# Kernel optimization log

Hardware: AMD Instinct MI355X
Metric: run time of the kernel (lower is better)

Reference implementation:

```python
import jax, jax.numpy as jnp
import numpy as np
import math


def setup_inputs() -> dict:
    key = jax.random.key(0)
    ks = jax.random.split(key, 8)
    B, S, dim = 4, 1024, 2048
    H, D = 16, 128          # n_heads = dim // core_dim
    T = 1024                # cached kv length
    w_scale = 1.0 / math.sqrt(dim)
    return {
        "x": jax.random.normal(ks[0], (B, S, dim), dtype=jnp.float32),
        "k_cache": jax.random.normal(ks[1], (B, H, T, D), dtype=jnp.float32),
        "v_cache": jax.random.normal(ks[2], (B, H, T, D), dtype=jnp.float32),
        "Wq": jax.random.normal(ks[3], (dim, dim), dtype=jnp.float32) * w_scale,
        "bq": jnp.zeros((dim,), jnp.float32),
        "Wk": jax.random.normal(ks[4], (dim, dim), dtype=jnp.float32) * w_scale,
        "bk": jnp.zeros((dim,), jnp.float32),
        "Wv": jax.random.normal(ks[5], (dim, dim), dtype=jnp.float32) * w_scale,
        "bv": jnp.zeros((dim,), jnp.float32),
        "Wo": jax.random.normal(ks[6], (dim, dim), dtype=jnp.float32) * w_scale,
        "bo": jnp.zeros((dim,), jnp.float32),
    }


def _split_heads(t, H):
    # [B, S, dim] -> [B, H, S, D]
    B, S, dim = t.shape
    return t.reshape(B, S, H, dim // H).transpose(0, 2, 1, 3)


def reference(x, k_cache, v_cache, Wq, bq, Wk, bk, Wv, bv, Wo, bo):
    B, S, dim = x.shape
    H = k_cache.shape[1]
    D = dim // H
    T = k_cache.shape[2]

    q = _split_heads(x @ Wq.T + bq, H)                 # [B,H,S,D]
    k_new = _split_heads(x @ Wk.T + bk, H)             # [B,H,S,D]
    v_new = _split_heads(x @ Wv.T + bv, H)

    k = jnp.concatenate([k_cache, k_new], axis=2)      # [B,H,T+S,D]
    v = jnp.concatenate([v_cache, v_new], axis=2)

    scale = 1.0 / math.sqrt(D)
    scores = jnp.einsum("bhqd,bhkd->bhqk", q, k) * scale   # [B,H,S,T+S]

    # causal mask with cache offset: query i may attend to key j iff j <= i + T
    q_pos = jnp.arange(S)[:, None] + T
    k_pos = jnp.arange(T + S)[None, :]
    mask = k_pos <= q_pos                              # [S, T+S]
    scores = jnp.where(mask[None, None], scores, jnp.finfo(scores.dtype).min)

    attn = jax.nn.softmax(scores, axis=-1)
    ctx = jnp.einsum("bhqk,bhkd->bhqd", attn, v)       # [B,H,S,D]
    ctx = ctx.transpose(0, 2, 1, 3).reshape(B, S, dim) # merge heads

    out = ctx @ Wo.T + bo                              # dropout is identity (p=0 / eval)
    return (out, k, v)
```

## Files before the change

kernel.cpp:

```cpp
#include <hip/hip_runtime.h>
#include <hip/hip_bf16.h>

typedef float f32x4 __attribute__((ext_vector_type(4)));
typedef __bf16 bf16x8 __attribute__((ext_vector_type(8)));
typedef unsigned short u16x8 __attribute__((ext_vector_type(8)));

#define DIMK 2048
#define QSCALE ((float)(0.08838834764831845 * 1.4426950408889634))

__device__ __forceinline__ unsigned short f2bf(float f) {
    union { float f; unsigned int u; } v; v.f = f;
    unsigned int r = v.u + 0x7fffu + ((v.u >> 16) & 1u);
    return (unsigned short)(r >> 16);
}
__device__ __forceinline__ float bf2f(unsigned short u) {
    union { unsigned int i; float f; } v; v.i = ((unsigned int)u) << 16; return v.f;
}

__device__ __forceinline__ void lds_load16(void* lds, const void* gsrc) {
    __builtin_amdgcn_global_load_lds(
        (const __attribute__((address_space(1))) unsigned int*)gsrc,
        (__attribute__((address_space(3))) unsigned int*)lds,
        16, 0, 0);
}


__global__ __launch_bounds__(256) void conv_all(
    const float* __restrict__ x,  const float* __restrict__ Wq,
    const float* __restrict__ Wk, const float* __restrict__ Wv,
    const float* __restrict__ Wo,
    unsigned short* __restrict__ xbf, unsigned short* __restrict__ Wqb,
    unsigned short* __restrict__ Wkb, unsigned short* __restrict__ Wvb,
    unsigned short* __restrict__ Wob)
{
    int i = blockIdx.x * 256 + threadIdx.x;
    const float* src; unsigned short* dst; size_t off;
    if (i < 2097152) { src = x; dst = xbf; off = i; }
    else {
        int j = (i - 2097152) >> 20;
        off = (size_t)((i - 2097152) & 1048575);
        src = j == 0 ? Wq : j == 1 ? Wk : j == 2 ? Wv : Wo;
        dst = j == 0 ? Wqb : j == 1 ? Wkb : j == 2 ? Wvb : Wob;
    }
    f32x4 v = *(const f32x4*)(src + off * 4);
    ushort4 pk = { f2bf(v[0]), f2bf(v[1]), f2bf(v[2]), f2bf(v[3]) };
    *(ushort4*)(dst + off * 4) = pk;
}

__global__ __launch_bounds__(256) void k_dual(
    const float* __restrict__ kc, float* __restrict__ kout, unsigned short* __restrict__ Kbf)
{
    size_t i4 = (size_t)blockIdx.x * 256 + threadIdx.x;
    size_t e = i4 * 4;
    size_t bh = e >> 17, rem = e & 131071;
    f32x4 v = *(const f32x4*)(kc + e);
    size_t dsto = (bh << 18) + rem;
    *(f32x4*)(kout + dsto) = v;
    ushort4 pk = { f2bf(v[0]), f2bf(v[1]), f2bf(v[2]), f2bf(v[3]) };
    *(ushort4*)(Kbf + dsto) = pk;
}

__global__ __launch_bounds__(256) void v_dual(
    const float* __restrict__ vc, float* __restrict__ vout, unsigned short* __restrict__ Vtb)
{
    __shared__ unsigned short T[128 * 72];
    const int kv0 = blockIdx.x * 64;
    const int bh = blockIdx.y;
    const int tid = threadIdx.x;
    const float* src = vc + ((size_t)bh << 17) + (size_t)kv0 * 128;
    float* vdst = vout + ((size_t)bh << 18) + (size_t)kv0 * 128;
    #pragma unroll
    for (int r = 0; r < 8; ++r) {
        int e4 = r * 256 + tid;
        int kv = e4 >> 5, d0 = (e4 & 31) << 2;
        f32x4 v = *(const f32x4*)(src + kv * 128 + d0);
        *(f32x4*)(vdst + kv * 128 + d0) = v;
        #pragma unroll
        for (int i = 0; i < 4; ++i) T[(d0 + i) * 72 + kv] = f2bf(v[i]);
    }
    __syncthreads();
    #pragma unroll
    for (int r = 0; r < 8; ++r) {
        int e = r * 256 + tid;
        int d = e >> 4, k4 = (e & 15) << 2;
        ushort4 pk = { T[d * 72 + k4], T[d * 72 + k4 + 1], T[d * 72 + k4 + 2], T[d * 72 + k4 + 3] };
        *(ushort4*)(Vtb + ((size_t)bh * 128 + d) * 2048 + kv0 + k4) = pk;
    }
}


#define GQ_TILE(T, VMC, DO_STAGE)                                                   \
    {                                                                               \
        const int bo = (T) & 3;                                                     \
        const unsigned short* la = LA + bo * 8192;                                  \
        const unsigned short* lb = LB + bo * 8192;                                  \
        bf16x8 af[4], bfj[4];                                                       \
        _Pragma("unroll")                                                           \
        for (int i = 0; i < 4; ++i)                                                 \
            af[i] = *(const bf16x8*)(la + (wr * 128 + i * 16 + c) * 32 + eoff);     \
        _Pragma("unroll")                                                           \
        for (int j = 0; j < 4; ++j)                                                 \
            bfj[j] = *(const bf16x8*)(lb + (wc * 64 + j * 16 + c) * 32 + eoff);     \
        if (DO_STAGE) {                                                             \
            const int sb = ((T) + 3) & 3;                                           \
            lds_load16(LA + sb * 8192 + w * 512, Asrc + ((T) + 3) * 32);            \
            lds_load16(LA + sb * 8192 + 4096 + w * 512, Asrc2 + ((T) + 3) * 32);    \
        }                                                                           \
        asm volatile("s_waitcnt lgkmcnt(0)" ::: "memory");                          \
        __builtin_amdgcn_sched_barrier(0);                                          \
        __builtin_amdgcn_s_setprio(1);                                              \
        _Pragma("unroll")                                                           \
        for (int i = 0; i < 4; ++i)                                                 \
            _Pragma("unroll")                                                       \
            for (int j = 0; j < 4; ++j)                                             \
                acc[i][j] = __builtin_amdgcn_mfma_f32_16x16x32_bf16(af[i], bfj[j], acc[i][j], 0, 0, 0); \
        __builtin_amdgcn_s_setprio(0);                                              \
        _Pragma("unroll")                                                           \
        for (int i = 0; i < 4; ++i)                                                 \
            af[i] = *(const bf16x8*)(la + (wr * 128 + 64 + i * 16 + c) * 32 + eoff);\
        if (DO_STAGE) {                                                             \
            const int sb = ((T) + 3) & 3;                                           \
            lds_load16(LB + sb * 8192 + w * 512, Bsrc + ((T) + 3) * 32);            \
            lds_load16(LB + sb * 8192 + 4096 + w * 512, Bsrc2 + ((T) + 3) * 32);    \
        }                                                                           \
        asm volatile("s_waitcnt vmcnt(" #VMC ")" ::: "memory");                     \
        asm volatile("s_waitcnt lgkmcnt(0)" ::: "memory");                          \
        __builtin_amdgcn_s_barrier();                                               \
        __builtin_amdgcn_sched_barrier(0);                                          \
        __builtin_amdgcn_s_setprio(1);                                              \
        _Pragma("unroll")                                                           \
        for (int i = 0; i < 4; ++i)                                                 \
            _Pragma("unroll")                                                       \
            for (int j = 0; j < 4; ++j)                                             \
                acc[4 + i][j] = __builtin_amdgcn_mfma_f32_16x16x32_bf16(af[i], bfj[j], acc[4 + i][j], 0, 0, 0); \
        __builtin_amdgcn_s_setprio(0);                                              \
    }

__device__ __forceinline__ void gemm_core256(
    const unsigned short* __restrict__ A16, const unsigned short* __restrict__ W16,
    int m0, int n0, unsigned short* LA, unsigned short* LB, f32x4 (&acc)[8][4],
    int tid, int w, int wr, int wc, int g, int c)
{
    const int srow = tid >> 2;
    const int achk = (tid & 3) ^ ((tid >> 3) & 3);
    const unsigned short* Asrc  = A16 + (size_t)(m0 + srow) * DIMK + achk * 8;
    const unsigned short* Asrc2 = A16 + (size_t)(m0 + 128 + srow) * DIMK + achk * 8;
    const unsigned short* Bsrc  = W16 + (size_t)(n0 + srow) * DIMK + achk * 8;
    const unsigned short* Bsrc2 = W16 + (size_t)(n0 + 128 + srow) * DIMK + achk * 8;
    const int eoff = (g ^ ((c >> 1) & 3)) * 8;

    #pragma unroll
    for (int ts = 0; ts < 3; ++ts) {
        lds_load16(LA + ts * 8192 + w * 512, Asrc + ts * 32);
        lds_load16(LA + ts * 8192 + 4096 + w * 512, Asrc2 + ts * 32);
        lds_load16(LB + ts * 8192 + w * 512, Bsrc + ts * 32);
        lds_load16(LB + ts * 8192 + 4096 + w * 512, Bsrc2 + ts * 32);
    }
    asm volatile("s_waitcnt vmcnt(8)" ::: "memory");
    __builtin_amdgcn_s_barrier();

    #pragma unroll 4
    for (int t = 0; t < 61; ++t)
        GQ_TILE(t, 8, true);
    GQ_TILE(61, 4, false);
    GQ_TILE(62, 0, false);
    GQ_TILE(63, 0, false);
}

__global__ __launch_bounds__(512, 2) void gemm_qkv256(
    const unsigned short* __restrict__ xbf,
    const unsigned short* __restrict__ Wqb, const unsigned short* __restrict__ Wkb,
    const unsigned short* __restrict__ Wvb,
    const float* __restrict__ bq, const float* __restrict__ bk, const float* __restrict__ bv,
    unsigned short* __restrict__ Qbf,
    float* __restrict__ kout, unsigned short* __restrict__ Kbf,
    float* __restrict__ vout, unsigned short* __restrict__ Vtb)
{
    const int o = blockIdx.x;
    const int xcd = o & 7;
    const int local = o >> 3;
    const int nloc = local >> 4;
    const int mblk = local & 15;
    const int nblk = xcd * 3 + nloc;
    const int m0 = mblk * 256;
    const int n0g = nblk * 256;
    const int mi = n0g >> 11;
    const int n0 = n0g & 2047;

    const unsigned short* W16 = mi == 0 ? Wqb : (mi == 1 ? Wkb : Wvb);
    const float* bias = mi == 0 ? bq : (mi == 1 ? bk : bv);

    const int tid = threadIdx.x;
    const int lane = tid & 63;
    const int w = tid >> 6;
    const int g = lane >> 4;
    const int c = lane & 15;
    const int wr = w >> 2, wc = w & 3;

    __shared__ unsigned short LA[4 * 8192];
    __shared__ unsigned short LB[4 * 8192];

    f32x4 acc[8][4];
    #pragma unroll
    for (int i = 0; i < 8; ++i)
        #pragma unroll
        for (int j = 0; j < 4; ++j)
            acc[i][j] = f32x4{0.f, 0.f, 0.f, 0.f};

    gemm_core256(xbf, W16, m0, n0, LA, LB, acc, tid, w, wr, wc, g, c);

    #pragma unroll
    for (int j = 0; j < 4; ++j) {
        const int n = n0 + wc * 64 + j * 16 + c;
        const float bn = bias[n];
        const int hh = n >> 7, d = n & 127;
        #pragma unroll
        for (int i = 0; i < 8; ++i) {
            float y4[4];
            #pragma unroll
            for (int tq = 0; tq < 4; ++tq) y4[tq] = acc[i][j][tq] + bn;
            const int mb = m0 + wr * 128 + i * 16 + g * 4;
            if (mi == 0) {
                #pragma unroll
                for (int tq = 0; tq < 4; ++tq) {
                    int m = mb + tq; int b = m >> 10, s = m & 1023;
                    Qbf[((((size_t)b * 16 + hh) << 10) + s) * 128 + d] = f2bf(y4[tq] * QSCALE);
                }
            } else if (mi == 1) {
                #pragma unroll
                for (int tq = 0; tq < 4; ++tq) {
                    int m = mb + tq; int b = m >> 10, s = m & 1023;
                    kout[(((size_t)b * 16 + hh) * 2048 + 1024 + s) * 128 + d] = y4[tq];
                    Kbf[(((size_t)b * 16 + hh) << 18) + (size_t)(1024 + s) * 128 + d] = f2bf(y4[tq]);
                }
            } else {
                #pragma unroll
                for (int tq = 0; tq < 4; ++tq) {
                    int m = mb + tq; int b = m >> 10, s = m & 1023;
                    vout[(((size_t)b * 16 + hh) * 2048 + 1024 + s) * 128 + d] = y4[tq];
                }
                int b = mb >> 10, s = mb & 1023;
                ushort4 pk = { f2bf(y4[0]), f2bf(y4[1]), f2bf(y4[2]), f2bf(y4[3]) };
                *(ushort4*)(Vtb + (((size_t)b * 16 + hh) * 128 + d) * 2048 + 1024 + s) = pk;
            }
        }
    }
}

__global__ __launch_bounds__(512, 2) void gemm_wo256(
    const unsigned short* __restrict__ ctx, const unsigned short* __restrict__ Wob,
    const float* __restrict__ bo, float* __restrict__ outp)
{
    const int o = blockIdx.x;
    const int xcd = o & 7;
    const int mblk = o >> 3;
    const int m0 = mblk * 256;
    const int n0 = xcd * 256;

    const int tid = threadIdx.x;
    const int lane = tid & 63;
    const int w = tid >> 6;
    const int g = lane >> 4;
    const int c = lane & 15;
    const int wr = w >> 2, wc = w & 3;

    __shared__ unsigned short LA[4 * 8192];
    __shared__ unsigned short LB[4 * 8192];

    f32x4 acc[8][4];
    #pragma unroll
    for (int i = 0; i < 8; ++i)
        #pragma unroll
        for (int j = 0; j < 4; ++j)
            acc[i][j] = f32x4{0.f, 0.f, 0.f, 0.f};

    gemm_core256(ctx, Wob, m0, n0, LA, LB, acc, tid, w, wr, wc, g, c);

    #pragma unroll
    for (int j = 0; j < 4; ++j) {
        const int n = n0 + wc * 64 + j * 16 + c;
        const float bn = bo[n];
        #pragma unroll
        for (int i = 0; i < 8; ++i) {
            const int mb = m0 + wr * 128 + i * 16 + g * 4;
            #pragma unroll
            for (int tq = 0; tq < 4; ++tq)
                outp[(size_t)(mb + tq) * 2048 + n] = acc[i][j][tq] + bn;
        }
    }
}

__global__ __launch_bounds__(256) void attn5(
    const unsigned short* __restrict__ Qbf,
    const unsigned short* __restrict__ Kbf,
    const unsigned short* __restrict__ Vtb,
    unsigned short* __restrict__ Pp,
    float* __restrict__ Mp,
    float* __restrict__ Lp)
{
    const int o = blockIdx.x;
    const int xcd = o & 7;
    const int kk0 = o >> 3;
    const int half = kk0 & 1;
    const int qt = 7 - ((kk0 >> 1) & 7);
    const int bh = (kk0 >> 4) * 8 + xcd;

    const int tid = threadIdx.x;
    const int lane = tid & 63;
    const int w = tid >> 6;
    const int g = lane >> 4;
    const int c = lane & 15;
    const int cswz = (c & 7) << 3;

    __shared__ unsigned short Ks[2][64 * 128];
    __shared__ unsigned short Vs[2][128 * 64];

    const unsigned short* Qb = Qbf + ((size_t)bh * 1024 + qt * 128) * 128;
    const unsigned short* Kb = Kbf + ((size_t)bh << 18);
    const unsigned short* Vt = Vtb + ((size_t)bh << 18);

    bf16x8 aq[2][4];
    #pragma unroll
    for (int m2 = 0; m2 < 2; ++m2)
        #pragma unroll
        for (int kd = 0; kd < 4; ++kd)
            aq[m2][kd] = *(const bf16x8*)(Qb + (w * 32 + m2 * 16 + c) * 128 + kd * 32 + g * 8);

    f32x4 od[2][8];
    #pragma unroll
    for (int m2 = 0; m2 < 2; ++m2)
        #pragma unroll
        for (int nf = 0; nf < 8; ++nf)
            od[m2][nf] = f32x4{0.f, 0.f, 0.f, 0.f};
    float mrow[2] = { -1e30f, -1e30f };
    float lrow[2] = { 0.f, 0.f };

    const int krow = tid >> 4;
    const int kswz = (((tid & 15) << 4) ^ ((krow & 7) << 4)) >> 1;
    const unsigned short* Kl = Kb + (size_t)krow * 128 + kswz;

    const int vd = tid >> 3;
    const int ck = tid & 7;
    const int kkv = ck >> 2;
    const int av = (ck >> 1) & 1;
    const int p0 = kkv * 32 + (((2 * ck) & 3) << 3) + av * 4;
    const int p1 = kkv * 32 + (((2 * ck + 1) & 3) << 3) + av * 4;

    const int cnt = 9 + qt;
    const int t0 = half * cnt;
    const int lim_min = 1024 + qt * 128 + w * 32;

    u16x8 vreg0, vreg1, vreg2, vreg3;

    {
        const int kv0 = t0 * 64;
        #pragma unroll
        for (int r = 0; r < 4; ++r)
            lds_load16(&Ks[0][w * 512 + r * 2048], Kl + (size_t)(kv0 + r * 16) * 128);
        vreg0 = *(const u16x8*)(Vt + (size_t)(vd +  0) * 2048 + kv0 + ck * 8);
        vreg1 = *(const u16x8*)(Vt + (size_t)(vd + 32) * 2048 + kv0 + ck * 8);
        vreg2 = *(const u16x8*)(Vt + (size_t)(vd + 64) * 2048 + kv0 + ck * 8);
        vreg3 = *(const u16x8*)(Vt + (size_t)(vd + 96) * 2048 + kv0 + ck * 8);
        #pragma unroll
        for (int r = 0; r < 4; ++r) {
            const int d = vd + r * 32;
            const int sw = (d & 7) << 3;
            unsigned short* row = &Vs[0][d * 64];
            u16x8 vv = r == 0 ? vreg0 : r == 1 ? vreg1 : r == 2 ? vreg2 : vreg3;
            ushort4 lo = { vv[0], vv[1], vv[2], vv[3] };
            ushort4 hi = { vv[4], vv[5], vv[6], vv[7] };
            *(ushort4*)(&row[p0 ^ sw]) = lo;
            *(ushort4*)(&row[p1 ^ sw]) = hi;
        }
        __syncthreads();
    }

    int cur = 0;
    for (int t = t0; t < t0 + cnt; ++t) {
        const int kv0 = t * 64;
        const bool next = (t + 1 < t0 + cnt);

        if (next) {
            const int kvn = kv0 + 64;
            #pragma unroll
            for (int r = 0; r < 4; ++r)
                lds_load16(&Ks[cur ^ 1][w * 512 + r * 2048], Kl + (size_t)(kvn + r * 16) * 128);
            vreg0 = *(const u16x8*)(Vt + (size_t)(vd +  0) * 2048 + kvn + ck * 8);
            vreg1 = *(const u16x8*)(Vt + (size_t)(vd + 32) * 2048 + kvn + ck * 8);
            vreg2 = *(const u16x8*)(Vt + (size_t)(vd + 64) * 2048 + kvn + ck * 8);
            vreg3 = *(const u16x8*)(Vt + (size_t)(vd + 96) * 2048 + kvn + ck * 8);
        }

        const unsigned short* Ksc = &Ks[cur][0];
        const unsigned short* Vsc = &Vs[cur][0];

        f32x4 sc[2][4];
        #pragma unroll
        for (int m2 = 0; m2 < 2; ++m2)
            #pragma unroll
            for (int n = 0; n < 4; ++n)
                sc[m2][n] = f32x4{0.f, 0.f, 0.f, 0.f};
        #pragma unroll
        for (int kd = 0; kd < 4; ++kd) {
            bf16x8 bk[4];
            #pragma unroll
            for (int n = 0; n < 4; ++n)
                bk[n] = *(const bf16x8*)(&Ksc[(n * 16 + c) * 128 + ((kd * 32 + g * 8) ^ cswz)]);
            #pragma unroll
            for (int m2 = 0; m2 < 2; ++m2)
                #pragma unroll
                for (int n = 0; n < 4; ++n)
                    sc[m2][n] = __builtin_amdgcn_mfma_f32_16x16x32_bf16(bk[n], aq[m2][kd], sc[m2][n], 0, 0, 0);
        }

        const bool need_mask = (kv0 + 63 > lim_min);
        #pragma unroll
        for (int m2 = 0; m2 < 2; ++m2) {
            if (need_mask) {
                const int lim = lim_min + m2 * 16 + c;
                #pragma unroll
                for (int n = 0; n < 4; ++n)
                    #pragma unroll
                    for (int j = 0; j < 4; ++j)
                        if (kv0 + n * 16 + g * 4 + j > lim) sc[m2][n][j] = -1e30f;
            }
            float rmax = sc[m2][0][0];
            #pragma unroll
            for (int n = 0; n < 4; ++n)
                #pragma unroll
                for (int j = 0; j < 4; ++j)
                    rmax = fmaxf(rmax, sc[m2][n][j]);
            rmax = fmaxf(rmax, __shfl_xor(rmax, 16));
            rmax = fmaxf(rmax, __shfl_xor(rmax, 32));

            if (!__all(rmax <= mrow[m2] + 8.0f)) {
                const float mnew = fmaxf(mrow[m2], rmax);
                const float fs = exp2f(mrow[m2] - mnew);
                mrow[m2] = mnew;
                lrow[m2] *= fs;
                #pragma unroll
                for (int j = 0; j < 4; ++j) {
                    const float fsj = __shfl(fs, (lane & 48) | (g * 4 + j));
                    #pragma unroll
                    for (int nf = 0; nf < 8; ++nf)
                        od[m2][nf][j] *= fsj;
                }
            }
            const float mm = mrow[m2];
            float rsum = 0.f;
            #pragma unroll
            for (int n = 0; n < 4; ++n)
                #pragma unroll
                for (int j = 0; j < 4; ++j) {
                    float p = exp2f(sc[m2][n][j] - mm);
                    sc[m2][n][j] = p;
                    rsum += p;
                }
            rsum += __shfl_xor(rsum, 16);
            rsum += __shfl_xor(rsum, 32);
            lrow[m2] += rsum;
        }

        if (next) {
            unsigned short* Vn = &Vs[cur ^ 1][0];
            #pragma unroll
            for (int r = 0; r < 4; ++r) {
                const int d = vd + r * 32;
                const int sw = (d & 7) << 3;
                unsigned short* row = &Vn[d * 64];
                u16x8 vv = r == 0 ? vreg0 : r == 1 ? vreg1 : r == 2 ? vreg2 : vreg3;
                ushort4 lo = { vv[0], vv[1], vv[2], vv[3] };
                ushort4 hi = { vv[4], vv[5], vv[6], vv[7] };
                *(ushort4*)(&row[p0 ^ sw]) = lo;
                *(ushort4*)(&row[p1 ^ sw]) = hi;
            }
        }

        union PA { u16x8 u; bf16x8 b; };
        PA pa[2][2];
        #pragma unroll
        for (int m2 = 0; m2 < 2; ++m2)
            #pragma unroll
            for (int kk = 0; kk < 2; ++kk)
                #pragma unroll
                for (int e = 0; e < 8; ++e)
                    pa[m2][kk].u[e] = f2bf(sc[m2][2 * kk + (e >> 2)][e & 3]);

        #pragma unroll
        for (int kk = 0; kk < 2; ++kk) {
            #pragma unroll
            for (int nf = 0; nf < 8; ++nf) {
                bf16x8 bv = *(const bf16x8*)(&Vsc[(nf * 16 + c) * 64 + ((kk * 32 + g * 8) ^ cswz)]);
                od[0][nf] = __builtin_amdgcn_mfma_f32_16x16x32_bf16(pa[0][kk].b, bv, od[0][nf], 0, 0, 0);
                od[1][nf] = __builtin_amdgcn_mfma_f32_16x16x32_bf16(pa[1][kk].b, bv, od[1][nf], 0, 0, 0);
            }
        }

        __syncthreads();
        cur ^= 1;
    }

    const size_t pbase = ((size_t)(half * 64 + bh) * 1024 + qt * 128) * 128;
    const int mlbase = (half * 64 + bh) * 1024 + qt * 128;
    if (lane < 16) {
        #pragma unroll
        for (int m2 = 0; m2 < 2; ++m2) {
            Mp[mlbase + w * 32 + m2 * 16 + c] = mrow[m2];
            Lp[mlbase + w * 32 + m2 * 16 + c] = lrow[m2];
        }
    }
    #pragma unroll
    for (int m2 = 0; m2 < 2; ++m2) {
        #pragma unroll
        for (int j = 0; j < 4; ++j) {
            const float lj = __shfl(lrow[m2], (lane & 48) | (g * 4 + j));
            const float rl = 1.0f / lj;
            const int ql = w * 32 + m2 * 16 + g * 4 + j;
            #pragma unroll
            for (int nf = 0; nf < 8; ++nf)
                Pp[pbase + (size_t)ql * 128 + nf * 16 + c] = f2bf(od[m2][nf][j] * rl);
        }
    }
}

__global__ __launch_bounds__(256) void merge_ctx(
    const unsigned short* __restrict__ Pp, const float* __restrict__ Mp,
    const float* __restrict__ Lp, unsigned short* __restrict__ ctx)
{
    const int idx = blockIdx.x * 256 + threadIdx.x;
    const int r = idx >> 4;
    const int dc = (idx & 15) << 3;
    const float m0 = Mp[r], m1 = Mp[65536 + r];
    const float l0 = Lp[r], l1 = Lp[65536 + r];
    const float M = fmaxf(m0, m1);
    float w0 = l0 * exp2f(m0 - M);
    float w1 = l1 * exp2f(m1 - M);
    const float inv = 1.0f / (w0 + w1);
    w0 *= inv; w1 *= inv;
    u16x8 a = *(const u16x8*)(Pp + (size_t)r * 128 + dc);
    u16x8 bb = *(const u16x8*)(Pp + (size_t)8388608 + (size_t)r * 128 + dc);
    const int bh = r >> 10, q = r & 1023;
    unsigned short* dst = ctx + ((size_t)(bh >> 4) * 1024 + q) * 2048 + (bh & 15) * 128 + dc;
    u16x8 outv;
    #pragma unroll
    for (int e = 0; e < 8; ++e)
        outv[e] = f2bf(w0 * bf2f(a[e]) + w1 * bf2f(bb[e]));
    *(u16x8*)dst = outv;
}

__global__ __launch_bounds__(256) void copy_cache(
    const float* __restrict__ kc, const float* __restrict__ vc,
    float* __restrict__ kout, float* __restrict__ vout)
{
    size_t i4 = (size_t)blockIdx.x * 256 + threadIdx.x;
    const float* src = blockIdx.y ? vc : kc;
    float* dst = blockIdx.y ? vout : kout;
    size_t e = i4 * 4;
    size_t bh = e >> 17, rem = e & 131071;
    f32x4 v = *(const f32x4*)(src + e);
    *(f32x4*)(dst + (bh << 18) + rem) = v;
}

template<int MODE, bool ABF16>
__global__ __launch_bounds__(256) void gemm_bt(
    const void* __restrict__ Ag, const float* __restrict__ Wf,
    const float* __restrict__ bias, void* __restrict__ dst)
{
    const int tid = threadIdx.x;
    const int lane = tid & 63;
    const int w = tid >> 6;
    const int g = lane >> 4;
    const int c = lane & 15;
    const int wr = w >> 1, wc = w & 1;
    const int m0 = blockIdx.y * 128;
    const int n0 = blockIdx.x * 128;

    __shared__ unsigned short As[128 * 40];
    __shared__ unsigned short Bs[128 * 40];

    f32x4 acc[4][4];
    #pragma unroll
    for (int i = 0; i < 4; ++i)
        #pragma unroll
        for (int j = 0; j < 4; ++j)
            acc[i][j] = f32x4{0.f, 0.f, 0.f, 0.f};

    for (int k0 = 0; k0 < DIMK; k0 += 32) {
        __syncthreads();
        if constexpr (ABF16) {
            const unsigned short* A16 = (const unsigned short*)Ag;
            #pragma unroll
            for (int r = 0; r < 2; ++r) {
                int e8 = r * 256 + tid;
                int row = e8 >> 2, col = (e8 & 3) << 3;
                *(uint4*)(&As[row * 40 + col]) =
                    *(const uint4*)(A16 + (size_t)(m0 + row) * DIMK + k0 + col);
            }
        } else {
            const float* Af = (const float*)Ag;
            #pragma unroll
            for (int r = 0; r < 4; ++r) {
                int e4 = r * 256 + tid;
                int row = e4 >> 3, col = (e4 & 7) << 2;
                f32x4 v = *(const f32x4*)(Af + (size_t)(m0 + row) * DIMK + k0 + col);
                ushort4 pk = { f2bf(v[0]), f2bf(v[1]), f2bf(v[2]), f2bf(v[3]) };
                *(ushort4*)(&As[row * 40 + col]) = pk;
            }
        }
        {
            #pragma unroll
            for (int r = 0; r < 4; ++r) {
                int e4 = r * 256 + tid;
                int row = e4 >> 3, col = (e4 & 7) << 2;
                f32x4 v = *(const f32x4*)(Wf + (size_t)(n0 + row) * DIMK + k0 + col);
                ushort4 pk = { f2bf(v[0]), f2bf(v[1]), f2bf(v[2]), f2bf(v[3]) };
                *(ushort4*)(&Bs[row * 40 + col]) = pk;
            }
        }
        __syncthreads();

        bf16x8 af[4], bfr[4];
        #pragma unroll
        for (int i = 0; i < 4; ++i)
            af[i] = *(const bf16x8*)(&As[(wr * 64 + i * 16 + c) * 40 + g * 8]);
        #pragma unroll
        for (int i = 0; i < 4; ++i)
            bfr[i] = *(const bf16x8*)(&Bs[(wc * 64 + i * 16 + c) * 40 + g * 8]);
        #pragma unroll
        for (int i = 0; i < 4; ++i)
            #pragma unroll
            for (int j = 0; j < 4; ++j)
                acc[i][j] = __builtin_amdgcn_mfma_f32_16x16x32_bf16(af[i], bfr[j], acc[i][j], 0, 0, 0);
    }

    #pragma unroll
    for (int j = 0; j < 4; ++j) {
        const int n = n0 + wc * 64 + j * 16 + c;
        const float bn = bias[n];
        #pragma unroll
        for (int i = 0; i < 4; ++i) {
            float y4[4];
            #pragma unroll
            for (int tq = 0; tq < 4; ++tq) y4[tq] = acc[i][j][tq] + bn;
            const int mb = m0 + wr * 64 + i * 16 + g * 4;
            if constexpr (MODE == 0) {
                #pragma unroll
                for (int tq = 0; tq < 4; ++tq) {
                    int m = mb + tq; int b = m >> 10, s = m & 1023;
                    int hh = n >> 7, d = n & 127;
                    ((unsigned short*)dst)[((((size_t)b * 16 + hh) << 10) + s) * 128 + d] = f2bf(y4[tq] * QSCALE);
                }
            } else if constexpr (MODE == 1) {
                #pragma unroll
                for (int tq = 0; tq < 4; ++tq) {
                    int m = mb + tq; int b = m >> 10, s = m & 1023;
                    int hh = n >> 7, d = n & 127;
                    ((float*)dst)[(((size_t)b * 16 + hh) * 2048 + 1024 + s) * 128 + d] = y4[tq];
                }
            } else {
                #pragma unroll
                for (int tq = 0; tq < 4; ++tq)
                    ((float*)dst)[(size_t)(mb + tq) * 2048 + n] = y4[tq];
            }
        }
    }
}

__global__ __launch_bounds__(256) void attn_stage(
    const unsigned short* __restrict__ Qbf,
    const float* __restrict__ Kf, const float* __restrict__ Vf,
    unsigned short* __restrict__ ctx)
{
    const int qt = blockIdx.x;
    const int bh = blockIdx.y;
    const int b = bh >> 4, h = bh & 15;
    const int tid = threadIdx.x;
    const int lane = tid & 63;
    const int w = tid >> 6;
    const int g = lane >> 4;
    const int c = lane & 15;

    __shared__ unsigned short Ksl[64 * 136];
    __shared__ unsigned short Vtl[128 * 72];
    __shared__ unsigned short Ps[4 * 32 * 72];

    bf16x8 aq[2][4];
    const unsigned short* Qb = Qbf + ((size_t)bh * 1024 + qt * 128) * 128;
    #pragma unroll
    for (int m2 = 0; m2 < 2; ++m2)
        #pragma unroll
        for (int kk = 0; kk < 4; ++kk)
            aq[m2][kk] = *(const bf16x8*)(Qb + (w * 32 + m2 * 16 + c) * 128 + kk * 32 + g * 8);

    f32x4 od[2][8];
    #pragma unroll
    for (int m2 = 0; m2 < 2; ++m2)
        #pragma unroll
        for (int nf = 0; nf < 8; ++nf)
            od[m2][nf] = f32x4{0.f, 0.f, 0.f, 0.f};
    float mrow[2][4], lrow[2][4];
    #pragma unroll
    for (int m2 = 0; m2 < 2; ++m2)
        #pragma unroll
        for (int j = 0; j < 4; ++j) { mrow[m2][j] = -1e30f; lrow[m2][j] = 0.f; }

    const float* Kb = Kf + (size_t)bh * 2048 * 128;
    const float* Vb = Vf + (size_t)bh * 2048 * 128;
    const int ntiles = 18 + 2 * qt;

    for (int t = 0; t < ntiles; ++t) {
        __syncthreads();
        const float* Kt = Kb + (size_t)t * 64 * 128;
        #pragma unroll
        for (int r = 0; r < 8; ++r) {
            int e4 = r * 256 + tid;
            int kv = e4 >> 5, d0 = (e4 & 31) << 2;
            f32x4 v = *(const f32x4*)(Kt + kv * 128 + d0);
            ushort4 pk = { f2bf(v[0]), f2bf(v[1]), f2bf(v[2]), f2bf(v[3]) };
            *(ushort4*)(&Ksl[kv * 136 + d0]) = pk;
        }
        const float* Vg = Vb + (size_t)t * 64 * 128;
        #pragma unroll
        for (int r = 0; r < 8; ++r) {
            int e4 = tid * 8 + r;
            int kv = e4 >> 5, d0 = (e4 & 31) << 2;
            f32x4 v = *(const f32x4*)(Vg + kv * 128 + d0);
            #pragma unroll
            for (int i = 0; i < 4; ++i)
                Vtl[(d0 + i) * 72 + kv] = f2bf(v[i]);
        }
        __syncthreads();

        f32x4 sc[2][4];
        #pragma unroll
        for (int m2 = 0; m2 < 2; ++m2)
            #pragma unroll
            for (int n = 0; n < 4; ++n)
                sc[m2][n] = f32x4{0.f, 0.f, 0.f, 0.f};
        #pragma unroll
        for (int kk = 0; kk < 4; ++kk) {
            bf16x8 bk[4];
            #pragma unroll
            for (int n = 0; n < 4; ++n)
                bk[n] = *(const bf16x8*)(&Ksl[(n * 16 + c) * 136 + kk * 32 + g * 8]);
            #pragma unroll
            for (int m2 = 0; m2 < 2; ++m2)
                #pragma unroll
                for (int n = 0; n < 4; ++n)
                    sc[m2][n] = __builtin_amdgcn_mfma_f32_16x16x32_bf16(aq[m2][kk], bk[n], sc[m2][n], 0, 0, 0);
        }

        const int kvbase = t * 64;
        #pragma unroll
        for (int m2 = 0; m2 < 2; ++m2) {
            #pragma unroll
            for (int j = 0; j < 4; ++j) {
                const int qg = qt * 128 + w * 32 + m2 * 16 + g * 4 + j;
                const int lim = qg + 1024;
                float rmax = -1e30f;
                #pragma unroll
                for (int n = 0; n < 4; ++n) {
                    float s = sc[m2][n][j] * QSCALE;
                    if (kvbase + n * 16 + c > lim) s = -1e30f;
                    sc[m2][n][j] = s;
                    rmax = fmaxf(rmax, s);
                }
                #pragma unroll
                for (int off = 1; off < 16; off <<= 1)
                    rmax = fmaxf(rmax, __shfl_xor(rmax, off));
                float mold = mrow[m2][j];
                float mnew = fmaxf(mold, rmax);
                mrow[m2][j] = mnew;
                float fs = exp2f(mold - mnew);
                float rsum = 0.f;
                #pragma unroll
                for (int n = 0; n < 4; ++n) {
                    float p = exp2f(sc[m2][n][j] - mnew);
                    sc[m2][n][j] = p;
                    rsum += p;
                }
                #pragma unroll
                for (int off = 1; off < 16; off <<= 1)
                    rsum += __shfl_xor(rsum, off);
                lrow[m2][j] = lrow[m2][j] * fs + rsum;
                #pragma unroll
                for (int nf = 0; nf < 8; ++nf)
                    od[m2][nf][j] *= fs;
            }
        }

        unsigned short* Pw = &Ps[w * 32 * 72];
        #pragma unroll
        for (int m2 = 0; m2 < 2; ++m2)
            #pragma unroll
            for (int n = 0; n < 4; ++n)
                #pragma unroll
                for (int j = 0; j < 4; ++j)
                    Pw[(m2 * 16 + g * 4 + j) * 72 + n * 16 + c] = f2bf(sc[m2][n][j]);

        #pragma unroll
        for (int kk = 0; kk < 2; ++kk) {
            bf16x8 ap0 = *(const bf16x8*)(&Ps[(w * 32 + c) * 72 + kk * 32 + g * 8]);
            bf16x8 ap1 = *(const bf16x8*)(&Ps[(w * 32 + 16 + c) * 72 + kk * 32 + g * 8]);
            #pragma unroll
            for (int nf = 0; nf < 8; ++nf) {
                bf16x8 bv = *(const bf16x8*)(&Vtl[(nf * 16 + c) * 72 + kk * 32 + g * 8]);
                od[0][nf] = __builtin_amdgcn_mfma_f32_16x16x32_bf16(ap0, bv, od[0][nf], 0, 0, 0);
                od[1][nf] = __builtin_amdgcn_mfma_f32_16x16x32_bf16(ap1, bv, od[1][nf], 0, 0, 0);
            }
        }
    }

    #pragma unroll
    for (int m2 = 0; m2 < 2; ++m2) {
        #pragma unroll
        for (int j = 0; j < 4; ++j) {
            const int qg = qt * 128 + w * 32 + m2 * 16 + g * 4 + j;
            const float rl = 1.0f / lrow[m2][j];
            #pragma unroll
            for (int nf = 0; nf < 8; ++nf) {
                const int d = nf * 16 + c;
                ctx[((size_t)b * 1024 + qg) * 2048 + h * 128 + d] = f2bf(od[m2][nf][j] * rl);
            }
        }
    }
}

extern "C" void kernel_launch(void* const* d_in, const int* in_sizes, int n_in,
                              void* d_out, int out_size, void* d_ws, size_t ws_size,
                              hipStream_t stream) {
    const float* x  = (const float*)d_in[0];
    const float* kc = (const float*)d_in[1];
    const float* vc = (const float*)d_in[2];
    const float* Wq = (const float*)d_in[3];
    const float* bq = (const float*)d_in[4];
    const float* Wk = (const float*)d_in[5];
    const float* bk = (const float*)d_in[6];
    const float* Wv = (const float*)d_in[7];
    const float* bv = (const float*)d_in[8];
    const float* Wo = (const float*)d_in[9];
    const float* bo = (const float*)d_in[10];

    float* outp = (float*)d_out;
    float* kout = outp + (size_t)8388608;
    float* vout = outp + (size_t)25165824;

    unsigned short* Qbf = (unsigned short*)d_ws;
    unsigned short* ctx = Qbf + (size_t)8388608;
    unsigned short* Kbf = ctx + (size_t)8388608;
    unsigned short* Vtb = Kbf + (size_t)16777216;
    unsigned short* xbf = Vtb + (size_t)16777216;
    unsigned short* Wqb = xbf + (size_t)8388608;
    unsigned short* Wkb = Wqb + (size_t)4194304;
    unsigned short* Wvb = Wkb + (size_t)4194304;
    unsigned short* Wob = Wvb + (size_t)4194304;
    unsigned short* Pp = xbf;
    float* Mp = (float*)Wvb;
    float* Lp = Mp + (size_t)131072;

    const bool full = ws_size >= (size_t)150994944;

    if (full) {
        conv_all<<<24576, 256, 0, stream>>>(x, Wq, Wk, Wv, Wo, xbf, Wqb, Wkb, Wvb, Wob);
        k_dual<<<8192, 256, 0, stream>>>(kc, kout, Kbf);
        v_dual<<<dim3(16, 64), 256, 0, stream>>>(vc, vout, Vtb);
        gemm_qkv256<<<384, 512, 0, stream>>>(xbf, Wqb, Wkb, Wvb, bq, bk, bv,
                                             Qbf, kout, Kbf, vout, Vtb);
        attn5<<<1024, 256, 0, stream>>>(Qbf, Kbf, Vtb, Pp, Mp, Lp);
        merge_ctx<<<4096, 256, 0, stream>>>(Pp, Mp, Lp, ctx);
        gemm_wo256<<<128, 512, 0, stream>>>(ctx, Wob, bo, outp);
    } else {
        copy_cache<<<dim3(8192, 2), 256, 0, stream>>>(kc, vc, kout, vout);
        gemm_bt<0, false><<<dim3(16, 32), 256, 0, stream>>>(x, Wq, bq, Qbf);
        gemm_bt<1, false><<<dim3(16, 32), 256, 0, stream>>>(x, Wk, bk, kout);
        gemm_bt<1, false><<<dim3(16, 32), 256, 0, stream>>>(x, Wv, bv, vout);
        attn_stage<<<dim3(8, 64), 256, 0, stream>>>(Qbf, kout, vout, ctx);
        gemm_bt<2, true><<<dim3(16, 32), 256, 0, stream>>>(ctx, Wo, bo, outp);
    }
}
```

Measured before the change: 454.0 us.

## Simplify GEMM pipeline to double buffering and drop split-KV attention merge

The 256-tile GEMM core goes from a 4-stage LDS ring with hand-placed waitcnts, setprio and barriers to a plain double-buffered loop with __syncthreads, which halves LDS use. The attention kernel no longer splits the KV range in two followed by a merge kernel. Each block now processes the full KV range for its query tile and writes normalized ctx directly. This removes the merge launch and its partial-result traffic, but halves the attention grid, makes per-block causal work uneven, and gives up the deeper GEMM prefetch and fine scheduling control.

```diff
diff --git a/kernel.cpp b/kernel.cpp
--- a/kernel.cpp
+++ b/kernel.cpp
@@ -88,55 +88,7 @@
     }
 }
 
-
-#define GQ_TILE(T, VMC, DO_STAGE)                                                   \
-    {                                                                               \
-        const int bo = (T) & 3;                                                     \
-        const unsigned short* la = LA + bo * 8192;                                  \
-        const unsigned short* lb = LB + bo * 8192;                                  \
-        bf16x8 af[4], bfj[4];                                                       \
-        _Pragma("unroll")                                                           \
-        for (int i = 0; i < 4; ++i)                                                 \
-            af[i] = *(const bf16x8*)(la + (wr * 128 + i * 16 + c) * 32 + eoff);     \
-        _Pragma("unroll")                                                           \
-        for (int j = 0; j < 4; ++j)                                                 \
-            bfj[j] = *(const bf16x8*)(lb + (wc * 64 + j * 16 + c) * 32 + eoff);     \
-        if (DO_STAGE) {                                                             \
-            const int sb = ((T) + 3) & 3;                                           \
-            lds_load16(LA + sb * 8192 + w * 512, Asrc + ((T) + 3) * 32);            \
-            lds_load16(LA + sb * 8192 + 4096 + w * 512, Asrc2 + ((T) + 3) * 32);    \
-        }                                                                           \
-        asm volatile("s_waitcnt lgkmcnt(0)" ::: "memory");                          \
-        __builtin_amdgcn_sched_barrier(0);                                          \
-        __builtin_amdgcn_s_setprio(1);                                              \
-        _Pragma("unroll")                                                           \
-        for (int i = 0; i < 4; ++i)                                                 \
-            _Pragma("unroll")                                                       \
-            for (int j = 0; j < 4; ++j)                                             \
-                acc[i][j] = __builtin_amdgcn_mfma_f32_16x16x32_bf16(af[i], bfj[j], acc[i][j], 0, 0, 0); \
-        __builtin_amdgcn_s_setprio(0);                                              \
-        _Pragma("unroll")                                                           \
-        for (int i = 0; i < 4; ++i)                                                 \
-            af[i] = *(const bf16x8*)(la + (wr * 128 + 64 + i * 16 + c) * 32 + eoff);\
-        if (DO_STAGE) {                                                             \
-            const int sb = ((T) + 3) & 3;                                           \
-            lds_load16(LB + sb * 8192 + w * 512, Bsrc + ((T) + 3) * 32);            \
-            lds_load16(LB + sb * 8192 + 4096 + w * 512, Bsrc2 + ((T) + 3) * 32);    \
-        }                                                                           \
-        asm volatile("s_waitcnt vmcnt(" #VMC ")" ::: "memory");                     \
-        asm volatile("s_waitcnt lgkmcnt(0)" ::: "memory");                          \
-        __builtin_amdgcn_s_barrier();                                               \
-        __builtin_amdgcn_sched_barrier(0);                                          \
-        __builtin_amdgcn_s_setprio(1);                                              \
-        _Pragma("unroll")                                                           \
-        for (int i = 0; i < 4; ++i)                                                 \
-            _Pragma("unroll")                                                       \
-            for (int j = 0; j < 4; ++j)                                             \
-                acc[4 + i][j] = __builtin_amdgcn_mfma_f32_16x16x32_bf16(af[i], bfj[j], acc[4 + i][j], 0, 0, 0); \
-        __builtin_amdgcn_s_setprio(0);                                              \
-    }
-
-__device__ __forceinline__ void gemm_core256(
+__device__ __forceinline__ void gemm_core256b(
     const unsigned short* __restrict__ A16, const unsigned short* __restrict__ W16,
     int m0, int n0, unsigned short* LA, unsigned short* LB, f32x4 (&acc)[8][4],
     int tid, int w, int wr, int wc, int g, int c)
@@ -149,22 +101,50 @@
     const unsigned short* Bsrc2 = W16 + (size_t)(n0 + 128 + srow) * DIMK + achk * 8;
     const int eoff = (g ^ ((c >> 1) & 3)) * 8;
 
-    #pragma unroll
-    for (int ts = 0; ts < 3; ++ts) {
-        lds_load16(LA + ts * 8192 + w * 512, Asrc + ts * 32);
-        lds_load16(LA + ts * 8192 + 4096 + w * 512, Asrc2 + ts * 32);
-        lds_load16(LB + ts * 8192 + w * 512, Bsrc + ts * 32);
-        lds_load16(LB + ts * 8192 + 4096 + w * 512, Bsrc2 + ts * 32);
-    }
-    asm volatile("s_waitcnt vmcnt(8)" ::: "memory");
-    __builtin_amdgcn_s_barrier();
-
-    #pragma unroll 4
-    for (int t = 0; t < 61; ++t)
-        GQ_TILE(t, 8, true);
-    GQ_TILE(61, 4, false);
-    GQ_TILE(62, 0, false);
-    GQ_TILE(63, 0, false);
+    lds_load16(LA + w * 512, Asrc);
+    lds_load16(LA + 4096 + w * 512, Asrc2);
+    lds_load16(LB + w * 512, Bsrc);
+    lds_load16(LB + 4096 + w * 512, Bsrc2);
+    __syncthreads();
+
+    #pragma unroll 2
+    for (int t = 0; t < 64; ++t) {
+        const int cur = t & 1;
+        const unsigned short* la = LA + cur * 8192;
+        const unsigned short* lb = LB + cur * 8192;
+
+        if (t + 1 < 64) {
+            const int nb = cur ^ 1;
+            lds_load16(LA + nb * 8192 + w * 512, Asrc + (t + 1) * 32);
+            lds_load16(LA + nb * 8192 + 4096 + w * 512, Asrc2 + (t + 1) * 32);
+            lds_load16(LB + nb * 8192 + w * 512, Bsrc + (t + 1) * 32);
+            lds_load16(LB + nb * 8192 + 4096 + w * 512, Bsrc2 + (t + 1) * 32);
+        }
+
+        bf16x8 af[4], af2[4], bfj[4];
+        #pragma unroll
+        for (int i = 0; i < 4; ++i)
+            af[i] = *(const bf16x8*)(la + (wr * 128 + i * 16 + c) * 32 + eoff);
+        #pragma unroll
+        for (int j = 0; j < 4; ++j)
+            bfj[j] = *(const bf16x8*)(lb + (wc * 64 + j * 16 + c) * 32 + eoff);
+        #pragma unroll
+        for (int i = 0; i < 4; ++i)
+            af2[i] = *(const bf16x8*)(la + (wr * 128 + 64 + i * 16 + c) * 32 + eoff);
+
+        #pragma unroll
+        for (int i = 0; i < 4; ++i)
+            #pragma unroll
+            for (int j = 0; j < 4; ++j)
+                acc[i][j] = __builtin_amdgcn_mfma_f32_16x16x32_bf16(af[i], bfj[j], acc[i][j], 0, 0, 0);
+        #pragma unroll
+        for (int i = 0; i < 4; ++i)
+            #pragma unroll
+            for (int j = 0; j < 4; ++j)
+                acc[4 + i][j] = __builtin_amdgcn_mfma_f32_16x16x32_bf16(af2[i], bfj[j], acc[4 + i][j], 0, 0, 0);
+
+        __syncthreads();
+    }
 }
 
 __global__ __launch_bounds__(512, 2) void gemm_qkv256(
@@ -197,8 +177,8 @@
     const int c = lane & 15;
     const int wr = w >> 2, wc = w & 3;
 
-    __shared__ unsigned short LA[4 * 8192];
-    __shared__ unsigned short LB[4 * 8192];
+    __shared__ unsigned short LA[2 * 8192];
+    __shared__ unsigned short LB[2 * 8192];
 
     f32x4 acc[8][4];
     #pragma unroll
@@ -207,7 +187,7 @@
         for (int j = 0; j < 4; ++j)
             acc[i][j] = f32x4{0.f, 0.f, 0.f, 0.f};
 
-    gemm_core256(xbf, W16, m0, n0, LA, LB, acc, tid, w, wr, wc, g, c);
+    gemm_core256b(xbf, W16, m0, n0, LA, LB, acc, tid, w, wr, wc, g, c);
 
     #pragma unroll
     for (int j = 0; j < 4; ++j) {
@@ -264,8 +244,8 @@
     const int c = lane & 15;
     const int wr = w >> 2, wc = w & 3;
 
-    __shared__ unsigned short LA[4 * 8192];
-    __shared__ unsigned short LB[4 * 8192];
+    __shared__ unsigned short LA[2 * 8192];
+    __shared__ unsigned short LB[2 * 8192];
 
     f32x4 acc[8][4];
     #pragma unroll
@@ -274,7 +254,7 @@
         for (int j = 0; j < 4; ++j)
             acc[i][j] = f32x4{0.f, 0.f, 0.f, 0.f};
 
-    gemm_core256(ctx, Wob, m0, n0, LA, LB, acc, tid, w, wr, wc, g, c);
+    gemm_core256b(ctx, Wob, m0, n0, LA, LB, acc, tid, w, wr, wc, g, c);
 
     #pragma unroll
     for (int j = 0; j < 4; ++j) {
@@ -290,20 +270,18 @@
     }
 }
 
-__global__ __launch_bounds__(256) void attn5(
+__global__ __launch_bounds__(256) void attn6(
     const unsigned short* __restrict__ Qbf,
     const unsigned short* __restrict__ Kbf,
     const unsigned short* __restrict__ Vtb,
-    unsigned short* __restrict__ Pp,
-    float* __restrict__ Mp,
-    float* __restrict__ Lp)
+    unsigned short* __restrict__ ctx)
 {
     const int o = blockIdx.x;
     const int xcd = o & 7;
-    const int kk0 = o >> 3;
-    const int half = kk0 & 1;
-    const int qt = 7 - ((kk0 >> 1) & 7);
-    const int bh = (kk0 >> 4) * 8 + xcd;
+    const int r2 = o >> 3;
+    const int qt = r2 & 7;
+    const int bh = (r2 >> 3) * 8 + xcd;
+    const int b = bh >> 4, h = bh & 15;
 
     const int tid = threadIdx.x;
     const int lane = tid & 63;
@@ -346,21 +324,19 @@
     const int p0 = kkv * 32 + (((2 * ck) & 3) << 3) + av * 4;
     const int p1 = kkv * 32 + (((2 * ck + 1) & 3) << 3) + av * 4;
 
-    const int cnt = 9 + qt;
-    const int t0 = half * cnt;
+    const int cnt = 18 + 2 * qt;
     const int lim_min = 1024 + qt * 128 + w * 32;
 
     u16x8 vreg0, vreg1, vreg2, vreg3;
 
     {
-        const int kv0 = t0 * 64;
         #pragma unroll
         for (int r = 0; r < 4; ++r)
-            lds_load16(&Ks[0][w * 512 + r * 2048], Kl + (size_t)(kv0 + r * 16) * 128);
-        vreg0 = *(const u16x8*)(Vt + (size_t)(vd +  0) * 2048 + kv0 + ck * 8);
-        vreg1 = *(const u16x8*)(Vt + (size_t)(vd + 32) * 2048 + kv0 + ck * 8);
-        vreg2 = *(const u16x8*)(Vt + (size_t)(vd + 64) * 2048 + kv0 + ck * 8);
-        vreg3 = *(const u16x8*)(Vt + (size_t)(vd + 96) * 2048 + kv0 + ck * 8);
+            lds_load16(&Ks[0][w * 512 + r * 2048], Kl + (size_t)(r * 16) * 128);
+        vreg0 = *(const u16x8*)(Vt + (size_t)(vd +  0) * 2048 + ck * 8);
+        vreg1 = *(const u16x8*)(Vt + (size_t)(vd + 32) * 2048 + ck * 8);
+        vreg2 = *(const u16x8*)(Vt + (size_t)(vd + 64) * 2048 + ck * 8);
+        vreg3 = *(const u16x8*)(Vt + (size_t)(vd + 96) * 2048 + ck * 8);
         #pragma unroll
         for (int r = 0; r < 4; ++r) {
             const int d = vd + r * 32;
@@ -376,9 +352,9 @@
     }
 
     int cur = 0;
-    for (int t = t0; t < t0 + cnt; ++t) {
+    for (int t = 0; t < cnt; ++t) {
         const int kv0 = t * 64;
-        const bool next = (t + 1 < t0 + cnt);
+        const bool next = (t + 1 < cnt);
 
         if (next) {
             const int kvn = kv0 + 64;
@@ -500,52 +476,20 @@
         cur ^= 1;
     }
 
-    const size_t pbase = ((size_t)(half * 64 + bh) * 1024 + qt * 128) * 128;
-    const int mlbase = (half * 64 + bh) * 1024 + qt * 128;
-    if (lane < 16) {
-        #pragma unroll
-        for (int m2 = 0; m2 < 2; ++m2) {
-            Mp[mlbase + w * 32 + m2 * 16 + c] = mrow[m2];
-            Lp[mlbase + w * 32 + m2 * 16 + c] = lrow[m2];
-        }
-    }
     #pragma unroll
     for (int m2 = 0; m2 < 2; ++m2) {
         #pragma unroll
         for (int j = 0; j < 4; ++j) {
             const float lj = __shfl(lrow[m2], (lane & 48) | (g * 4 + j));
             const float rl = 1.0f / lj;
-            const int ql = w * 32 + m2 * 16 + g * 4 + j;
-            #pragma unroll
-            for (int nf = 0; nf < 8; ++nf)
-                Pp[pbase + (size_t)ql * 128 + nf * 16 + c] = f2bf(od[m2][nf][j] * rl);
-        }
-    }
-}
-
-__global__ __launch_bounds__(256) void merge_ctx(
-    const unsigned short* __restrict__ Pp, const float* __restrict__ Mp,
-    const float* __restrict__ Lp, unsigned short* __restrict__ ctx)
-{
-    const int idx = blockIdx.x * 256 + threadIdx.x;
-    const int r = idx >> 4;
-    const int dc = (idx & 15) << 3;
-    const float m0 = Mp[r], m1 = Mp[65536 + r];
-    const float l0 = Lp[r], l1 = Lp[65536 + r];
-    const float M = fmaxf(m0, m1);
-    float w0 = l0 * exp2f(m0 - M);
-    float w1 = l1 * exp2f(m1 - M);
-    const float inv = 1.0f / (w0 + w1);
-    w0 *= inv; w1 *= inv;
-    u16x8 a = *(const u16x8*)(Pp + (size_t)r * 128 + dc);
-    u16x8 bb = *(const u16x8*)(Pp + (size_t)8388608 + (size_t)r * 128 + dc);
-    const int bh = r >> 10, q = r & 1023;
-    unsigned short* dst = ctx + ((size_t)(bh >> 4) * 1024 + q) * 2048 + (bh & 15) * 128 + dc;
-    u16x8 outv;
-    #pragma unroll
-    for (int e = 0; e < 8; ++e)
-        outv[e] = f2bf(w0 * bf2f(a[e]) + w1 * bf2f(bb[e]));
-    *(u16x8*)dst = outv;
+            const int qg = qt * 128 + w * 32 + m2 * 16 + g * 4 + j;
+            #pragma unroll
+            for (int nf = 0; nf < 8; ++nf) {
+                const int d = nf * 16 + c;
+                ctx[((size_t)b * 1024 + qg) * 2048 + h * 128 + d] = f2bf(od[m2][nf][j] * rl);
+            }
+        }
+    }
 }
 
 __global__ __launch_bounds__(256) void copy_cache(
@@ -854,9 +798,6 @@
     unsigned short* Wkb = Wqb + (size_t)4194304;
     unsigned short* Wvb = Wkb + (size_t)4194304;
     unsigned short* Wob = Wvb + (size_t)4194304;
-    unsigned short* Pp = xbf;
-    float* Mp = (float*)Wvb;
-    float* Lp = Mp + (size_t)131072;
 
     const bool full = ws_size >= (size_t)150994944;
 
@@ -866,8 +807,7 @@
         v_dual<<<dim3(16, 64), 256, 0, stream>>>(vc, vout, Vtb);
         gemm_qkv256<<<384, 512, 0, stream>>>(xbf, Wqb, Wkb, Wvb, bq, bk, bv,
                                              Qbf, kout, Kbf, vout, Vtb);
-        attn5<<<1024, 256, 0, stream>>>(Qbf, Kbf, Vtb, Pp, Mp, Lp);
-        merge_ctx<<<4096, 256, 0, stream>>>(Pp, Mp, Lp, ctx);
+        attn6<<<512, 256, 0, stream>>>(Qbf, Kbf, Vtb, ctx);
         gemm_wo256<<<128, 512, 0, stream>>>(ctx, Wob, bo, outp);
     } else {
         copy_cache<<<dim3(8192, 2), 256, 0, stream>>>(kc, vc, kout, vout);
```

New measurement: 481.9 us. 1.06x slower.
